# Optimization experiments

Hardware: AMD Instinct MI355X
Metric: run time of the kernel (lower is better)

Reference implementation:

```python
import jax, jax.numpy as jnp
import numpy as np

B, M, C, IMG, P, D, L, H, DFF, NC = 16, 4, 3, 224, 16, 768, 12, 12, 3072, 1000
G = IMG // P
S = G * G + 1
HD = D // H
EPS = 1e-6
SCALE = HD ** -0.5


def setup_inputs() -> dict:
    key = jax.random.key(0)
    ks = jax.random.split(key, 12)
    w = lambda k, shape: (jax.random.normal(k, shape) * 0.02).astype(jnp.float32)
    return {
        'x': jax.random.normal(ks[0], (B, C, IMG, IMG), jnp.float32),
        'x_tangent': jax.random.normal(ks[1], (B, M, C, IMG, IMG), jnp.float32),
        'patch_w': w(ks[2], (D, C * P * P)), 'patch_b': jnp.zeros((D,), jnp.float32),
        'cls_token': w(ks[3], (1, 1, D)), 'pos_embed': w(ks[4], (1, S, D)),
        'ln1_g': jnp.ones((L, D), jnp.float32), 'ln1_b': jnp.zeros((L, D), jnp.float32),
        'qkv_w': w(ks[5], (L, 3 * D, D)), 'qkv_b': jnp.zeros((L, 3 * D), jnp.float32),
        'proj_w': w(ks[6], (L, D, D)), 'proj_b': jnp.zeros((L, D), jnp.float32),
        'ln2_g': jnp.ones((L, D), jnp.float32), 'ln2_b': jnp.zeros((L, D), jnp.float32),
        'fc1_w': w(ks[7], (L, DFF, D)), 'fc1_b': jnp.zeros((L, DFF), jnp.float32),
        'fc2_w': w(ks[8], (L, D, DFF)), 'fc2_b': jnp.zeros((L, D), jnp.float32),
        'normf_g': jnp.ones((D,), jnp.float32), 'normf_b': jnp.zeros((D,), jnp.float32),
        'head_w': w(ks[9], (NC, D)), 'head_b': jnp.zeros((NC,), jnp.float32),
    }


def _patchify(img):
    # [b,C,IMG,IMG] -> [b, G*G, C*P*P], matching Conv2d(patch) weight layout (c, ph, pw)
    b = img.shape[0]
    p = img.reshape(b, C, G, P, G, P).transpose(0, 2, 4, 1, 3, 5)
    return p.reshape(b, G * G, C * P * P)


def _ln_jvp(x, t, g, b):
    # x: [B,S,D], t: [B,M,S,D]; params constant w.r.t. tangent directions
    mu = x.mean(-1, keepdims=True)
    xc = x - mu
    inv = jax.lax.rsqrt((xc * xc).mean(-1, keepdims=True) + EPS)
    xh = xc * inv
    y = xh * g + b
    xh_b, inv_b = xh[:, None], inv[:, None]
    ty = g * inv_b * (t - t.mean(-1, keepdims=True) - xh_b * (xh_b * t).mean(-1, keepdims=True))
    return y, ty


def _gelu_jvp(x, t):
    # exact (erf) GELU and its derivative; x: [B,S,F], t: [B,M,S,F]
    cdf = 0.5 * (1.0 + jax.lax.erf(x * 0.7071067811865476))
    pdf = jnp.exp(-0.5 * x * x) * 0.3989422804014327
    return x * cdf, t * (cdf + x * pdf)[:, None]


def _softmax_jvp(s, ts):
    # s: [B,H,S,S], ts: [B,M,H,S,S]
    a = jax.nn.softmax(s, axis=-1)
    a_b = a[:, None]
    ta = a_b * (ts - (a_b * ts).sum(-1, keepdims=True))
    return a, ta


def reference(x, x_tangent, patch_w, patch_b, cls_token, pos_embed,
              ln1_g, ln1_b, qkv_w, qkv_b, proj_w, proj_b, ln2_g, ln2_b,
              fc1_w, fc1_b, fc2_w, fc2_b, normf_g, normf_b, head_w, head_b):
    # patch embed (primal + tangent; bias/pos/cls are constants -> zero tangent)
    h = _patchify(x) @ patch_w.T + patch_b                                  # [B,N,D]
    th = (_patchify(x_tangent.reshape(B * M, C, IMG, IMG)) @ patch_w.T).reshape(B, M, G * G, D)
    cls = jnp.broadcast_to(cls_token, (B, 1, D))
    h = jnp.concatenate([cls, h], axis=1) + pos_embed                       # [B,S,D]
    th = jnp.concatenate([jnp.zeros((B, M, 1, D), th.dtype), th], axis=2)   # [B,M,S,D]

    for l in range(L):
        # --- attention (manual JVP, matching the torch einsum path) ---
        y, ty = _ln_jvp(h, th, ln1_g[l], ln1_b[l])
        qkv = y @ qkv_w[l].T + qkv_b[l]
        tqkv = ty @ qkv_w[l].T
        q, k, v = jnp.split(qkv, 3, axis=-1)
        tq, tk, tv = jnp.split(tqkv, 3, axis=-1)
        q = q.reshape(B, S, H, HD); k = k.reshape(B, S, H, HD); v = v.reshape(B, S, H, HD)
        tq = tq.reshape(B, M, S, H, HD); tk = tk.reshape(B, M, S, H, HD); tv = tv.reshape(B, M, S, H, HD)
        s = jnp.einsum('bqhd,bkhd->bhqk', q, k) * SCALE
        ts = (jnp.einsum('bmqhd,bkhd->bmhqk', tq, k)
              + jnp.einsum('bqhd,bmkhd->bmhqk', q, tk)) * SCALE
        a, ta = _softmax_jvp(s, ts)
        o = jnp.einsum('bhqk,bkhd->bqhd', a, v).reshape(B, S, D)
        to = (jnp.einsum('bmhqk,bkhd->bmqhd', ta, v)
              + jnp.einsum('bhqk,bmkhd->bmqhd', a, tv)).reshape(B, M, S, D)
        h = h + o @ proj_w[l].T + proj_b[l]
        th = th + to @ proj_w[l].T
        # --- mlp ---
        y, ty = _ln_jvp(h, th, ln2_g[l], ln2_b[l])
        y = y @ fc1_w[l].T + fc1_b[l]
        ty = ty @ fc1_w[l].T
        y, ty = _gelu_jvp(y, ty)
        h = h + y @ fc2_w[l].T + fc2_b[l]
        th = th + ty @ fc2_w[l].T

    y, ty = _ln_jvp(h, th, normf_g, normf_b)
    logits = y[:, 0] @ head_w.T + head_b            # token pooling
    tlogits = ty[:, :, 0] @ head_w.T                 # [B,M,NC]
    return logits, tlogits
```

## Files before the change

### kernel.cpp

```cpp
#include <hip/hip_runtime.h>
#include <hip/hip_bf16.h>

#define DEVI __device__ __forceinline__

typedef short  bf16x8 __attribute__((ext_vector_type(8)));
typedef float  f32x4  __attribute__((ext_vector_type(4)));

static constexpr int BB   = 16;
static constexpr int MM   = 4;
static constexpr int CC   = 3;
static constexpr int IMG  = 224;
static constexpr int PPP  = 16;
static constexpr int DD   = 768;
static constexpr int LL   = 12;
static constexpr int HH   = 12;
static constexpr int DFF  = 3072;
static constexpr int NCLS = 1000;
static constexpr int GG   = 14;
static constexpr int SS   = 197;
static constexpr int HD   = 64;
static constexpr int BT   = BB*SS;
static constexpr int BMT  = BB*MM*SS;
static constexpr int RT   = BT+BMT;
static constexpr int RP   = 15872;
static constexpr int SP   = 208;
static constexpr int QLD  = 3*DD;
static constexpr int PRP  = BB*GG*GG;
static constexpr int PRT  = (BB+BB*MM)*GG*GG;
static constexpr float EPSV  = 1e-6f;
static constexpr float SCALE = 0.125f;

static constexpr int NQW  = QLD*DD;
static constexpr int NPW  = DD*DD;
static constexpr int NF1W = DFF*DD;
static constexpr int NF2W = DD*DFF;
static constexpr int WTOT = NQW+NPW+NF1W+NF2W;

static constexpr int CH   = 4;
static constexpr int BMC  = (BB*MM)/CH;

DEVI unsigned short f2bf(float x){
  union { float f; unsigned u; } v; v.f = x;
  unsigned r = v.u + 0x7fffu + ((v.u>>16)&1u);
  return (unsigned short)(r>>16);
}
DEVI float bf2f(unsigned short x){
  union { unsigned u; float f; } v; v.u = ((unsigned)x)<<16;
  return v.f;
}
DEVI f32x4 mfma16(bf16x8 a, bf16x8 b, f32x4 c){
  return __builtin_amdgcn_mfma_f32_16x16x32_bf16(a,b,c,0,0,0);
}
typedef const void __attribute__((address_space(1)))* gas1;
typedef void __attribute__((address_space(3)))* las3;


__global__ __launch_bounds__(256) void f2bf_kernel(const float* __restrict__ in,
    unsigned short* __restrict__ out, size_t n){
  size_t i = (size_t)blockIdx.x*256 + threadIdx.x;
  size_t stride = (size_t)gridDim.x*256;
  for (; i<n; i+=stride) out[i] = f2bf(in[i]);
}

__global__ __launch_bounds__(256) void conv_layer(const float* __restrict__ qkvw,
    const float* __restrict__ projw, const float* __restrict__ f1w,
    const float* __restrict__ f2w, unsigned short* __restrict__ wl){
  int i = blockIdx.x*256 + threadIdx.x;
  float v;
  if (i < NQW)                v = qkvw[i];
  else if (i < NQW+NPW)       v = projw[i-NQW];
  else if (i < NQW+NPW+NF1W)  v = f1w[i-NQW-NPW];
  else                        v = f2w[i-NQW-NPW-NF1W];
  wl[i] = f2bf(v);
}

__global__ __launch_bounds__(256) void init_h(float* __restrict__ hh,
    const float* __restrict__ cls, const float* __restrict__ pos,
    const float* __restrict__ patch_b){
  size_t i = (size_t)blockIdx.x*256 + threadIdx.x;
  int r = (int)(i/DD), c = (int)(i%DD);
  float v = 0.f;
  if (r < BT){
    int s_ = r % SS;
    v = pos[(size_t)s_*DD + c] + (s_==0 ? cls[c] : patch_b[c]);
  }
  hh[i] = v;
}

__global__ __launch_bounds__(256) void patchify_k(const float* __restrict__ x,
    const float* __restrict__ xt, unsigned short* __restrict__ pat){
  size_t i = (size_t)blockIdx.x*256 + threadIdx.x;
  int r = (int)(i/DD), kk = (int)(i%DD);
  int c = kk>>8, rem = kk&255, py = rem>>4, px = rem&15;
  const float* src;
  if (r < PRP){
    int b_ = r/(GG*GG), p = r%(GG*GG);
    src = x + (((size_t)b_*CC + c)*IMG + (size_t)(p/GG)*PPP + py)*IMG + (p%GG)*PPP + px;
  } else {
    int rr = r-PRP; int bm = rr/(GG*GG), p = rr%(GG*GG);
    src = xt + (((size_t)bm*CC + c)*IMG + (size_t)(p/GG)*PPP + py)*IMG + (p%GG)*PPP + px;
  }
  pat[i] = f2bf(*src);
}


DEVI float blockSum256(float v, float* red){
  #pragma unroll
  for (int off=32; off; off>>=1) v += __shfl_xor(v, off, 64);
  int wave = threadIdx.x>>6;
  if ((threadIdx.x&63)==0) red[wave] = v;
  __syncthreads();
  float r = red[0]+red[1]+red[2]+red[3];
  __syncthreads();
  return r;
}

__global__ __launch_bounds__(256) void ln_primal(const float* __restrict__ hh,
    const float* __restrict__ g, const float* __restrict__ bb,
    unsigned short* __restrict__ ybf, float* __restrict__ stats){
  __shared__ float red[4];
  int r = blockIdx.x;
  const float* x = hh + (size_t)r*DD;
  int t = threadIdx.x;
  float x0=x[t], x1=x[t+256], x2=x[t+512];
  float mu = blockSum256(x0+x1+x2, red) * (1.f/DD);
  float d0=x0-mu, d1=x1-mu, d2=x2-mu;
  float var = blockSum256(d0*d0+d1*d1+d2*d2, red) * (1.f/DD);
  float inv = rsqrtf(var + EPSV);
  unsigned short* y = ybf + (size_t)r*DD;
  y[t]     = f2bf(d0*inv*g[t]     + bb[t]);
  y[t+256] = f2bf(d1*inv*g[t+256] + bb[t+256]);
  y[t+512] = f2bf(d2*inv*g[t+512] + bb[t+512]);
  if (t==0){ stats[2*r]=mu; stats[2*r+1]=inv; }
}

__global__ __launch_bounds__(256) void ln_tangent(const float* __restrict__ hh,
    const float* __restrict__ g, unsigned short* __restrict__ ybf,
    const float* __restrict__ stats){
  __shared__ float red[4];
  int r = blockIdx.x;
  int gr = BT + r;
  int s_ = r % SS;
  int b_ = (r / SS) / MM;
  int pr = b_*SS + s_;
  const float* tt = hh + (size_t)gr*DD;
  const float* xx = hh + (size_t)pr*DD;
  float mu = stats[2*pr], inv = stats[2*pr+1];
  int t = threadIdx.x;
  float t0=tt[t], t1=tt[t+256], t2=tt[t+512];
  float h0=(xx[t]-mu)*inv, h1=(xx[t+256]-mu)*inv, h2=(xx[t+512]-mu)*inv;
  float tmean = blockSum256(t0+t1+t2, red)*(1.f/DD);
  float dot   = blockSum256(h0*t0+h1*t1+h2*t2, red)*(1.f/DD);
  unsigned short* y = ybf + (size_t)gr*DD;
  y[t]     = f2bf(g[t]    *inv*(t0 - tmean - h0*dot));
  y[t+256] = f2bf(g[t+256]*inv*(t1 - tmean - h1*dot));
  y[t+512] = f2bf(g[t+512]*inv*(t2 - tmean - h2*dot));
}


template<int MODE>
__global__ __launch_bounds__(256,2) void gemm_bt(
    const unsigned short* __restrict__ A,
    const unsigned short* __restrict__ Aalt, int asplit, int lda,
    const unsigned short* __restrict__ W, int K, int N, int Mrows,
    float* __restrict__ outf, unsigned short* __restrict__ outb, int ldc,
    const float* __restrict__ bias, int bias_limit)
{
  __shared__ __attribute__((aligned(16))) unsigned short As[128*64];
  __shared__ __attribute__((aligned(16))) unsigned short Bs[128*64];
  const int tid = threadIdx.x;
  const int wave = tid>>6, lane = tid&63;
  const int tM = blockIdx.y, tN = blockIdx.x;
  f32x4 acc[4][4];
  f32x4 zf = {0.f,0.f,0.f,0.f};
  #pragma unroll
  for (int m=0;m<4;m++)
    #pragma unroll
    for (int n=0;n<4;n++) acc[m][n] = zf;
  const int wm = wave>>1, wn = wave&1;
  const int lrow = lane&15, lk8 = (lane>>4)<<3;
  const int srow = tid>>3;
  const int scol = (tid&7)<<3;
  const size_t arow0 = (size_t)tM*128;
  const size_t brow0 = (size_t)tN*128;

  for (int k0=0; k0<K; k0+=64){
    #pragma unroll
    for (int i=0;i<4;i++){
      int row = (int)arow0 + srow + i*32;
      const unsigned short* abase = (row < asplit) ? Aalt : A;
      const unsigned short* ga = abase + (size_t)row*lda + (k0+scol);
      __builtin_amdgcn_global_load_lds((gas1)ga, (las3)(As + i*2048 + wave*512), 16, 0, 0);
      const unsigned short* gb = W + (brow0+srow+i*32)*(size_t)K + (k0+scol);
      __builtin_amdgcn_global_load_lds((gas1)gb, (las3)(Bs + i*2048 + wave*512), 16, 0, 0);
    }
    __syncthreads();
    #pragma unroll
    for (int kk=0; kk<64; kk+=32){
      bf16x8 af[4], bw[4];
      #pragma unroll
      for (int m=0;m<4;m++) af[m] = *(const bf16x8*)(As + (wm*64+m*16+lrow)*64 + kk+lk8);
      #pragma unroll
      for (int n=0;n<4;n++) bw[n] = *(const bf16x8*)(Bs + (wn*64+n*16+lrow)*64 + kk+lk8);
      #pragma unroll
      for (int m=0;m<4;m++)
        #pragma unroll
        for (int n=0;n<4;n++)
          acc[m][n] = mfma16(af[m], bw[n], acc[m][n]);
    }
    __syncthreads();
  }

  const int colbase = tN*128 + wn*64 + lrow;
  const int rowbase = tM*128 + wm*64 + ((lane>>4)<<2);
  #pragma unroll
  for (int n=0;n<4;n++){
    int col = colbase + n*16;
    #pragma unroll
    for (int m=0;m<4;m++){
      #pragma unroll
      for (int i=0;i<4;i++){
        int r = rowbase + m*16 + i;
        float v = acc[m][n][i];
        if (MODE==0){
          if (r < bias_limit) v += bias[col];
          outb[(size_t)r*ldc + col] = f2bf(v);
        } else if (MODE==1){
          if (r < Mrows){
            if (r < bias_limit) v += bias[col];
            outf[(size_t)r*ldc + col] += v;
          }
        } else {
          if (r < PRT){
            int orow;
            if (r < PRP) orow = (r/196)*197 + 1 + r%196;
            else { int rr = r-PRP; orow = BT + (rr/196)*197 + 1 + rr%196; }
            outf[(size_t)orow*ldc + col] += v;
          }
        }
      }
    }
  }
}

__global__ __launch_bounds__(256) void transpose_v(const unsigned short* __restrict__ qkv,
    unsigned short* __restrict__ vT, unsigned short* __restrict__ tvT){
  __shared__ unsigned short tile[SP*65];
  int inst = blockIdx.x;
  size_t rowbase; unsigned short* dst; int h;
  if (inst < BB*HH){ int b_=inst/HH; h=inst%HH; rowbase=(size_t)b_*SS; dst = vT + (size_t)inst*HD*SP; }
  else { int i2=inst-BB*HH; int bm=i2/HH; h=i2%HH; rowbase=(size_t)BT+(size_t)bm*SS; dst = tvT + (size_t)i2*HD*SP; }
  int coff = 2*DD + h*HD;
  for (int i=threadIdx.x; i<SP*HD; i+=256){
    int k = i>>6, d = i&63;
    unsigned short v = (k<SS) ? qkv[(rowbase+k)*QLD + coff + d] : (unsigned short)0;
    tile[k*65+d] = v;
  }
  __syncthreads();
  for (int i=threadIdx.x; i<HD*SP; i+=256){
    int d = i/SP, k = i%SP;
    dst[(size_t)d*SP + k] = tile[k*65+d];
  }
}

__global__ __launch_bounds__(256) void attn_s1(const unsigned short* __restrict__ qkv,
                                               unsigned short* __restrict__ abf){
  int qt = blockIdx.x, inst = blockIdx.y;
  int wave = threadIdx.x>>6, lane = threadIdx.x&63;
  int lrow = lane&15, lk = (lane>>4)<<3;
  int q0 = qt*64 + wave*16;
  f32x4 acc[13];
  f32x4 zf = {0.f,0.f,0.f,0.f};
  #pragma unroll
  for (int n=0;n<13;n++) acc[n]=zf;
  int h = inst % HH, b_ = inst / HH;
  size_t prow = (size_t)b_*SS;
  const unsigned short* Ab = qkv + (prow + q0 + lrow)*QLD + h*HD + lk;
  const unsigned short* Bb = qkv + prow*QLD + DD + h*HD + lk;
  #pragma unroll
  for (int kk=0; kk<HD; kk+=32){
    bf16x8 av = *(const bf16x8*)(Ab + kk);
    #pragma unroll
    for (int n=0;n<13;n++){
      bf16x8 bv = *(const bf16x8*)(Bb + (size_t)(n*16+lrow)*QLD + kk);
      acc[n] = mfma16(av, bv, acc[n]);
    }
  }
  int grp = lane>>4;
  unsigned short* obase = abf + (size_t)inst*SP*SP;
  bool okc12 = (lrow < 5);
  #pragma unroll
  for (int i=0;i<4;i++){
    int qr = q0 + grp*4 + i;
    float val[13], e[13];
    float mv = -1e30f;
    #pragma unroll
    for (int n=0;n<13;n++){
      val[n] = acc[n][i]*SCALE;
      if (n<12 || okc12) mv = fmaxf(mv, val[n]);
    }
    #pragma unroll
    for (int off=8; off; off>>=1) mv = fmaxf(mv, __shfl_xor(mv, off, 64));
    float s = 0.f;
    #pragma unroll
    for (int n=0;n<13;n++){
      e[n] = (n<12 || okc12) ? __expf(val[n]-mv) : 0.f;
      s += e[n];
    }
    #pragma unroll
    for (int off=8; off; off>>=1) s += __shfl_xor(s, off, 64);
    float inv = 1.f/s;
    if (qr < SS){
      unsigned short* orow = obase + (size_t)qr*SP;
      #pragma unroll
      for (int n=0;n<13;n++) orow[n*16+lrow] = f2bf(e[n]*inv);
    }
  }
}

__global__ __launch_bounds__(256) void attn_s2(const unsigned short* __restrict__ qkv,
    const unsigned short* __restrict__ abf, unsigned short* __restrict__ tabf,
    int bmix0){
  int qt = blockIdx.x, il = blockIdx.y;
  int wave = threadIdx.x>>6, lane = threadIdx.x&63;
  int lrow = lane&15, lk = (lane>>4)<<3;
  int q0 = qt*64 + wave*16;
  f32x4 acc[13];
  f32x4 zf = {0.f,0.f,0.f,0.f};
  #pragma unroll
  for (int n=0;n<13;n++) acc[n]=zf;
  int h = il % HH;
  int bmix = bmix0 + il / HH;
  int b_ = bmix / MM;
  int bh = b_*HH + h;
  size_t prow = (size_t)b_*SS;
  size_t trow = (size_t)BT + (size_t)bmix*SS;
  #pragma unroll
  for (int p=0;p<2;p++){
    size_t ar = (p==0) ? trow : prow;
    size_t br = (p==1) ? trow : prow;
    const unsigned short* Ab = qkv + (ar + q0 + lrow)*QLD + h*HD + lk;
    const unsigned short* Bb = qkv + br*QLD + DD + h*HD + lk;
    #pragma unroll
    for (int kk=0; kk<HD; kk+=32){
      bf16x8 av = *(const bf16x8*)(Ab + kk);
      #pragma unroll
      for (int n=0;n<13;n++){
        bf16x8 bv = *(const bf16x8*)(Bb + (size_t)(n*16+lrow)*QLD + kk);
        acc[n] = mfma16(av, bv, acc[n]);
      }
    }
  }
  int grp = lane>>4;
  const unsigned short* abase = abf + (size_t)bh*SP*SP;
  unsigned short* tbase = tabf + (size_t)il*SP*SP;
  #pragma unroll
  for (int i=0;i<4;i++){
    int qr = q0 + grp*4 + i;
    int qc = (qr < SS) ? qr : (SS-1);
    const unsigned short* arow = abase + (size_t)qc*SP;
    float av[13], tv[13];
    float dot = 0.f;
    #pragma unroll
    for (int n=0;n<13;n++){
      tv[n] = acc[n][i]*SCALE;
      av[n] = bf2f(arow[n*16+lrow]);
      dot += av[n]*tv[n];
    }
    #pragma unroll
    for (int off=8; off; off>>=1) dot += __shfl_xor(dot, off, 64);
    if (qr < SS){
      unsigned short* trow_ = tbase + (size_t)qr*SP;
      #pragma unroll
      for (int n=0;n<13;n++) trow_[n*16+lrow] = f2bf(av[n]*(tv[n]-dot));
    }
  }
}

template<int NP>
__global__ __launch_bounds__(256) void attn_pv(
    const unsigned short* __restrict__ abf, const unsigned short* __restrict__ tabf,
    const unsigned short* __restrict__ vT,  const unsigned short* __restrict__ tvT,
    unsigned short* __restrict__ obf, int bmix0){
  int qt = blockIdx.x, il = blockIdx.y;
  int wave = threadIdx.x>>6, lane = threadIdx.x&63;
  int lrow = lane&15, lk = (lane>>4)<<3;
  int q0 = qt*64 + wave*16;
  int h = il % HH;
  int bmix = (NP==1) ? (il/HH) : (bmix0 + il/HH);
  int b_ = (NP==1) ? bmix : bmix/MM;
  int bh = b_*HH + h;
  f32x4 acc[4];
  f32x4 zf = {0.f,0.f,0.f,0.f};
  #pragma unroll
  for (int n=0;n<4;n++) acc[n]=zf;
  int arow = q0 + lrow; if (arow > SP-1) arow = SP-1;
  #pragma unroll
  for (int p=0;p<NP;p++){
    const unsigned short* Ab = (NP==2 && p==0) ? tabf + (size_t)il*SP*SP
                                               : abf + (size_t)bh*SP*SP;
    const unsigned short* Bb = (NP==2 && p==1) ? tvT + (size_t)(bmix*HH+h)*HD*SP
                                               : vT + (size_t)bh*HD*SP;
    #pragma unroll
    for (int ks=0; ks<6; ks++){
      int kb = ks*32 + lk;
      bf16x8 av = *(const bf16x8*)(Ab + (size_t)arow*SP + kb);
      #pragma unroll
      for (int n=0;n<4;n++){
        bf16x8 bv = *(const bf16x8*)(Bb + (size_t)(n*16+lrow)*SP + kb);
        acc[n] = mfma16(av, bv, acc[n]);
      }
    }
    {
      int kb = 192 + lk;
      const bf16x8 ZV = {0,0,0,0,0,0,0,0};
      bool ok = (lk < 16);
      bf16x8 av = ok ? *(const bf16x8*)(Ab + (size_t)arow*SP + kb) : ZV;
      #pragma unroll
      for (int n=0;n<4;n++){
        bf16x8 bv = ok ? *(const bf16x8*)(Bb + (size_t)(n*16+lrow)*SP + kb) : ZV;
        acc[n] = mfma16(av, bv, acc[n]);
      }
    }
  }
  size_t orow0 = (NP==1) ? (size_t)bmix*SS : (size_t)BT + (size_t)bmix*SS;
  int qr0 = q0 + ((lane>>4)<<2);
  #pragma unroll
  for (int n=0;n<4;n++){
    int cc = h*HD + n*16 + lrow;
    #pragma unroll
    for (int i=0;i<4;i++){
      int qr = qr0 + i;
      if (qr < SS) obf[(orow0+qr)*DD + cc] = f2bf(acc[n][i]);
    }
  }
}

__global__ __launch_bounds__(256) void gelu_k(unsigned short* __restrict__ fc1o,
                                              unsigned short* __restrict__ pgbf){
  int r = blockIdx.x;
  bool prim = r < BT;
  int pr = 0;
  if (!prim){ int idx = r-BT; int s_ = idx%SS; int b_ = (idx/SS)/MM; pr = b_*SS + s_; }
  size_t base  = (size_t)r*DFF;
  size_t pbase = (size_t)pr*DFF;
  for (int c=threadIdx.x; c<DFF; c+=256){
    if (prim){
      float x = bf2f(fc1o[base+c]);
      float cdf = 0.5f*(1.f + erff(x*0.70710678118654752f));
      pgbf[base+c] = f2bf(x*cdf);
    } else {
      float tv = bf2f(fc1o[base+c]);
      float x  = bf2f(fc1o[pbase+c]);
      float cdf = 0.5f*(1.f + erff(x*0.70710678118654752f));
      float pdf = __expf(-0.5f*x*x)*0.39894228040143267f;
      fc1o[base+c] = f2bf(tv*(cdf + x*pdf));
    }
  }
}

__global__ __launch_bounds__(256) void head_k(const unsigned short* __restrict__ ybf,
    const float* __restrict__ hw, const float* __restrict__ hb, float* __restrict__ out){
  __shared__ float ysh[DD];
  int ri = blockIdx.x;
  size_t yrow; float* o; bool wb;
  if (ri < BB){ yrow = (size_t)ri*SS; o = out + (size_t)ri*NCLS; wb = true; }
  else { int t2 = ri-BB; yrow = (size_t)BT + (size_t)t2*SS; o = out + (size_t)BB*NCLS + (size_t)t2*NCLS; wb = false; }
  for (int d=threadIdx.x; d<DD; d+=256) ysh[d] = bf2f(ybf[yrow*DD + d]);
  __syncthreads();
  for (int n=threadIdx.x; n<NCLS; n+=256){
    const float* wrow = hw + (size_t)n*DD;
    float acc = wb ? hb[n] : 0.f;
    for (int d=0; d<DD; d++) acc += ysh[d]*wrow[d];
    o[n] = acc;
  }
}

extern "C" void kernel_launch(void* const* d_in, const int* in_sizes, int n_in,
                              void* d_out, int out_size, void* d_ws, size_t ws_size,
                              hipStream_t stream)
{
  const float* x      = (const float*)d_in[0];
  const float* xt     = (const float*)d_in[1];
  const float* patch_w= (const float*)d_in[2];
  const float* patch_b= (const float*)d_in[3];
  const float* cls    = (const float*)d_in[4];
  const float* pos    = (const float*)d_in[5];
  const float* ln1_g  = (const float*)d_in[6];
  const float* ln1_b  = (const float*)d_in[7];
  const float* qkv_w  = (const float*)d_in[8];
  const float* qkv_b  = (const float*)d_in[9];
  const float* proj_w = (const float*)d_in[10];
  const float* proj_b = (const float*)d_in[11];
  const float* ln2_g  = (const float*)d_in[12];
  const float* ln2_b  = (const float*)d_in[13];
  const float* fc1_w  = (const float*)d_in[14];
  const float* fc1_b  = (const float*)d_in[15];
  const float* fc2_w  = (const float*)d_in[16];
  const float* fc2_b  = (const float*)d_in[17];
  const float* nf_g   = (const float*)d_in[18];
  const float* nf_b   = (const float*)d_in[19];
  const float* head_w = (const float*)d_in[20];
  const float* head_b = (const float*)d_in[21];
  float* out = (float*)d_out;

  char* ws = (char*)d_ws;
  size_t off = 0;
  auto alloc = [&](size_t bytes)->char*{
    char* p = ws + off;
    off = (off + bytes + 255) & ~(size_t)255;
    return p;
  };
  unsigned short* w_patch = (unsigned short*)alloc((size_t)DD*DD*2);
  unsigned short* wl      = (unsigned short*)alloc((size_t)WTOT*2);
  float* hh            = (float*)alloc((size_t)RP*DD*4);
  unsigned short* ybf  = (unsigned short*)alloc((size_t)RP*DD*2);
  float* stats         = (float*)alloc((size_t)BT*2*4);
  size_t slab0 = off;
  unsigned short* qkvbf= (unsigned short*)alloc((size_t)RP*QLD*2);
  unsigned short* vT   = (unsigned short*)alloc((size_t)BB*HH*HD*SP*2);
  unsigned short* tvT  = (unsigned short*)alloc((size_t)BB*MM*HH*HD*SP*2);
  unsigned short* abf  = (unsigned short*)alloc((size_t)BB*HH*SP*SP*2);
  unsigned short* tabf = (unsigned short*)alloc((size_t)BMC*HH*SP*SP*2);
  size_t endA = off;
  off = slab0;
  unsigned short* fc1o = (unsigned short*)alloc((size_t)RP*DFF*2);
  unsigned short* pgbf = (unsigned short*)alloc((size_t)BT*DFF*2);
  size_t endB = off;
  size_t need = (endA > endB) ? endA : endB;

  if (need > ws_size){
    hipMemsetAsync(d_out, 0x7f, (size_t)out_size*4, stream);
    return;
  }

  dim3 blk(256);
  f2bf_kernel<<<dim3(2304), blk, 0, stream>>>(patch_w, w_patch, (size_t)DD*DD);
  init_h<<<dim3((RP*DD)/256), blk, 0, stream>>>(hh, cls, pos, patch_b);
  patchify_k<<<dim3((PRT*DD)/256), blk, 0, stream>>>(x, xt, ybf);
  gemm_bt<2><<<dim3(DD/128, 123), blk, 0, stream>>>(ybf, nullptr, 0, DD, w_patch, DD, DD, PRT,
                                                    hh, nullptr, DD, nullptr, 0);

  unsigned short* w_qkv = wl;
  unsigned short* w_proj= wl + NQW;
  unsigned short* w_fc1 = wl + NQW + NPW;
  unsigned short* w_fc2 = wl + NQW + NPW + NF1W;

  for (int l=0; l<LL; l++){
    conv_layer<<<dim3(WTOT/256), blk, 0, stream>>>(qkv_w+(size_t)l*NQW, proj_w+(size_t)l*NPW,
                                                   fc1_w+(size_t)l*NF1W, fc2_w+(size_t)l*NF2W, wl);
    ln_primal <<<dim3(BT),  blk, 0, stream>>>(hh, ln1_g+(size_t)l*DD, ln1_b+(size_t)l*DD, ybf, stats);
    ln_tangent<<<dim3(BMT), blk, 0, stream>>>(hh, ln1_g+(size_t)l*DD, ybf, stats);
    gemm_bt<0><<<dim3(QLD/128, RP/128), blk, 0, stream>>>(ybf, nullptr, 0, DD, w_qkv,
        DD, QLD, RT, nullptr, qkvbf, QLD, qkv_b+(size_t)l*QLD, BT);
    transpose_v<<<dim3(BB*HH + BB*MM*HH), blk, 0, stream>>>(qkvbf, vT, tvT);
    attn_s1<<<dim3(4, BB*HH), blk, 0, stream>>>(qkvbf, abf);
    attn_pv<1><<<dim3(4, BB*HH), blk, 0, stream>>>(abf, nullptr, vT, nullptr, ybf, 0);
    for (int c=0; c<CH; c++){
      attn_s2<<<dim3(4, BMC*HH), blk, 0, stream>>>(qkvbf, abf, tabf, c*BMC);
      attn_pv<2><<<dim3(4, BMC*HH), blk, 0, stream>>>(abf, tabf, vT, tvT, ybf, c*BMC);
    }
    gemm_bt<1><<<dim3(DD/128, RP/128), blk, 0, stream>>>(ybf, nullptr, 0, DD, w_proj,
        DD, DD, RT, hh, nullptr, DD, proj_b+(size_t)l*DD, BT);
    ln_primal <<<dim3(BT),  blk, 0, stream>>>(hh, ln2_g+(size_t)l*DD, ln2_b+(size_t)l*DD, ybf, stats);
    ln_tangent<<<dim3(BMT), blk, 0, stream>>>(hh, ln2_g+(size_t)l*DD, ybf, stats);
    gemm_bt<0><<<dim3(DFF/128, RP/128), blk, 0, stream>>>(ybf, nullptr, 0, DD, w_fc1,
        DD, DFF, RT, nullptr, fc1o, DFF, fc1_b+(size_t)l*DFF, BT);
    gelu_k<<<dim3(RT), blk, 0, stream>>>(fc1o, pgbf);
    gemm_bt<1><<<dim3(DD/128, RP/128), blk, 0, stream>>>(fc1o, pgbf, BT, DFF, w_fc2,
        DFF, DD, RT, hh, nullptr, DD, fc2_b+(size_t)l*DD, BT);
  }

  ln_primal <<<dim3(BT),  blk, 0, stream>>>(hh, nf_g, nf_b, ybf, stats);
  ln_tangent<<<dim3(BMT), blk, 0, stream>>>(hh, nf_g, ybf, stats);
  head_k<<<dim3(BB + BB*MM), blk, 0, stream>>>(ybf, head_w, head_b, out);
}
```

Measured before the change: 8.521 ms.

## Fuse layernorm kernels, convert all weights upfront, remap GEMM tiles per XCD, vectorize GELU

Primal and tangent layernorm are merged into one launch that recomputes the primal statistics per row with a single four-way block reduction, so the stats buffer and the second launch go away. All layers' weights are converted to bf16 in one kernel when the workspace is large enough, so the per-layer conversion launch is skipped. GEMM workgroup IDs are remapped so that consecutive tiles land on the same XCD, which is meant to improve L2 reuse. GELU is vectorized to 8-wide bf16 accesses, and the final layernorm only processes the rows the head reads. The one-pass variance (E[x^2] - mu^2) is less numerically robust, and converting every layer's weights up front takes more workspace memory.

```diff
diff --git a/kernel.cpp b/kernel.cpp
--- a/kernel.cpp
+++ b/kernel.cpp
@@ -74,6 +74,19 @@
   wl[i] = f2bf(v);
 }
 
+__global__ __launch_bounds__(256) void conv_all(const float* __restrict__ qkvw,
+    const float* __restrict__ projw, const float* __restrict__ f1w,
+    const float* __restrict__ f2w, unsigned short* __restrict__ wl){
+  int l = blockIdx.y;
+  int i = blockIdx.x*256 + threadIdx.x;
+  float v;
+  if (i < NQW)                v = qkvw[(size_t)l*NQW + i];
+  else if (i < NQW+NPW)       v = projw[(size_t)l*NPW + (i-NQW)];
+  else if (i < NQW+NPW+NF1W)  v = f1w[(size_t)l*NF1W + (i-NQW-NPW)];
+  else                        v = f2w[(size_t)l*NF2W + (i-NQW-NPW-NF1W)];
+  wl[(size_t)l*WTOT + i] = f2bf(v);
+}
+
 __global__ __launch_bounds__(256) void init_h(float* __restrict__ hh,
     const float* __restrict__ cls, const float* __restrict__ pos,
     const float* __restrict__ patch_b){
@@ -104,57 +117,99 @@
 }
 
 
-DEVI float blockSum256(float v, float* red){
-  #pragma unroll
-  for (int off=32; off; off>>=1) v += __shfl_xor(v, off, 64);
-  int wave = threadIdx.x>>6;
-  if ((threadIdx.x&63)==0) red[wave] = v;
+DEVI void blockSum4(float&a,float&b,float&c,float&d,float* red){
+  #pragma unroll
+  for (int off=32; off; off>>=1){
+    a += __shfl_xor(a,off,64); b += __shfl_xor(b,off,64);
+    c += __shfl_xor(c,off,64); d += __shfl_xor(d,off,64);
+  }
+  int w = threadIdx.x>>6;
+  if ((threadIdx.x&63)==0){ red[w]=a; red[4+w]=b; red[8+w]=c; red[12+w]=d; }
   __syncthreads();
-  float r = red[0]+red[1]+red[2]+red[3];
+  a = red[0]+red[1]+red[2]+red[3];
+  b = red[4]+red[5]+red[6]+red[7];
+  c = red[8]+red[9]+red[10]+red[11];
+  d = red[12]+red[13]+red[14]+red[15];
   __syncthreads();
-  return r;
-}
-
-__global__ __launch_bounds__(256) void ln_primal(const float* __restrict__ hh,
+}
+
+__global__ __launch_bounds__(256) void ln_fused(const float* __restrict__ hh,
     const float* __restrict__ g, const float* __restrict__ bb,
-    unsigned short* __restrict__ ybf, float* __restrict__ stats){
-  __shared__ float red[4];
+    unsigned short* __restrict__ ybf){
+  __shared__ float red[16];
   int r = blockIdx.x;
-  const float* x = hh + (size_t)r*DD;
   int t = threadIdx.x;
-  float x0=x[t], x1=x[t+256], x2=x[t+512];
-  float mu = blockSum256(x0+x1+x2, red) * (1.f/DD);
-  float d0=x0-mu, d1=x1-mu, d2=x2-mu;
-  float var = blockSum256(d0*d0+d1*d1+d2*d2, red) * (1.f/DD);
-  float inv = rsqrtf(var + EPSV);
   unsigned short* y = ybf + (size_t)r*DD;
-  y[t]     = f2bf(d0*inv*g[t]     + bb[t]);
-  y[t+256] = f2bf(d1*inv*g[t+256] + bb[t+256]);
-  y[t+512] = f2bf(d2*inv*g[t+512] + bb[t+512]);
-  if (t==0){ stats[2*r]=mu; stats[2*r+1]=inv; }
-}
-
-__global__ __launch_bounds__(256) void ln_tangent(const float* __restrict__ hh,
-    const float* __restrict__ g, unsigned short* __restrict__ ybf,
-    const float* __restrict__ stats){
-  __shared__ float red[4];
-  int r = blockIdx.x;
-  int gr = BT + r;
-  int s_ = r % SS;
-  int b_ = (r / SS) / MM;
-  int pr = b_*SS + s_;
-  const float* tt = hh + (size_t)gr*DD;
-  const float* xx = hh + (size_t)pr*DD;
-  float mu = stats[2*pr], inv = stats[2*pr+1];
+  if (r < BT){
+    const float* x = hh + (size_t)r*DD;
+    float x0=x[t], x1=x[t+256], x2=x[t+512];
+    float s1=x0+x1+x2, s2=x0*x0+x1*x1+x2*x2, s3=0.f, s4=0.f;
+    blockSum4(s1,s2,s3,s4,red);
+    float mu  = s1*(1.f/DD);
+    float inv = rsqrtf(s2*(1.f/DD) - mu*mu + EPSV);
+    y[t]     = f2bf((x0-mu)*inv*g[t]     + bb[t]);
+    y[t+256] = f2bf((x1-mu)*inv*g[t+256] + bb[t+256]);
+    y[t+512] = f2bf((x2-mu)*inv*g[t+512] + bb[t+512]);
+  } else {
+    int idx = r-BT;
+    int s_ = idx % SS;
+    int b_ = (idx / SS) / MM;
+    int pr = b_*SS + s_;
+    const float* tt = hh + (size_t)r*DD;
+    const float* xx = hh + (size_t)pr*DD;
+    float t0=tt[t], t1=tt[t+256], t2=tt[t+512];
+    float x0=xx[t], x1=xx[t+256], x2=xx[t+512];
+    float s1=x0+x1+x2, s2=x0*x0+x1*x1+x2*x2;
+    float s3=t0+t1+t2, s4=x0*t0+x1*t1+x2*t2;
+    blockSum4(s1,s2,s3,s4,red);
+    float mu  = s1*(1.f/DD);
+    float inv = rsqrtf(s2*(1.f/DD) - mu*mu + EPSV);
+    float tmean = s3*(1.f/DD);
+    float dot   = inv*(s4*(1.f/DD) - mu*tmean);
+    y[t]     = f2bf(g[t]    *inv*(t0 - tmean - (x0-mu)*inv*dot));
+    y[t+256] = f2bf(g[t+256]*inv*(t1 - tmean - (x1-mu)*inv*dot));
+    y[t+512] = f2bf(g[t+512]*inv*(t2 - tmean - (x2-mu)*inv*dot));
+  }
+}
+
+__global__ __launch_bounds__(256) void ln_head(const float* __restrict__ hh,
+    const float* __restrict__ g, const float* __restrict__ bb,
+    unsigned short* __restrict__ ybf){
+  __shared__ float red[16];
+  int ri = blockIdx.x;
   int t = threadIdx.x;
-  float t0=tt[t], t1=tt[t+256], t2=tt[t+512];
-  float h0=(xx[t]-mu)*inv, h1=(xx[t+256]-mu)*inv, h2=(xx[t+512]-mu)*inv;
-  float tmean = blockSum256(t0+t1+t2, red)*(1.f/DD);
-  float dot   = blockSum256(h0*t0+h1*t1+h2*t2, red)*(1.f/DD);
-  unsigned short* y = ybf + (size_t)gr*DD;
-  y[t]     = f2bf(g[t]    *inv*(t0 - tmean - h0*dot));
-  y[t+256] = f2bf(g[t+256]*inv*(t1 - tmean - h1*dot));
-  y[t+512] = f2bf(g[t+512]*inv*(t2 - tmean - h2*dot));
+  if (ri < BB){
+    size_t row = (size_t)ri*SS;
+    const float* x = hh + row*DD;
+    float x0=x[t], x1=x[t+256], x2=x[t+512];
+    float s1=x0+x1+x2, s2=x0*x0+x1*x1+x2*x2, s3=0.f, s4=0.f;
+    blockSum4(s1,s2,s3,s4,red);
+    float mu  = s1*(1.f/DD);
+    float inv = rsqrtf(s2*(1.f/DD) - mu*mu + EPSV);
+    unsigned short* y = ybf + row*DD;
+    y[t]     = f2bf((x0-mu)*inv*g[t]     + bb[t]);
+    y[t+256] = f2bf((x1-mu)*inv*g[t+256] + bb[t+256]);
+    y[t+512] = f2bf((x2-mu)*inv*g[t+512] + bb[t+512]);
+  } else {
+    int t2 = ri - BB;
+    size_t row = (size_t)BT + (size_t)t2*SS;
+    size_t prow = (size_t)(t2/MM)*SS;
+    const float* tt = hh + row*DD;
+    const float* xx = hh + prow*DD;
+    float t0=tt[t], t1=tt[t+256], t2v=tt[t+512];
+    float x0=xx[t], x1=xx[t+256], x2=xx[t+512];
+    float s1=x0+x1+x2, s2=x0*x0+x1*x1+x2*x2;
+    float s3=t0+t1+t2v, s4=x0*t0+x1*t1+x2*t2v;
+    blockSum4(s1,s2,s3,s4,red);
+    float mu  = s1*(1.f/DD);
+    float inv = rsqrtf(s2*(1.f/DD) - mu*mu + EPSV);
+    float tmean = s3*(1.f/DD);
+    float dot   = inv*(s4*(1.f/DD) - mu*tmean);
+    unsigned short* y = ybf + row*DD;
+    y[t]     = f2bf(g[t]    *inv*(t0  - tmean - (x0-mu)*inv*dot));
+    y[t+256] = f2bf(g[t+256]*inv*(t1  - tmean - (x1-mu)*inv*dot));
+    y[t+512] = f2bf(g[t+512]*inv*(t2v - tmean - (x2-mu)*inv*dot));
+  }
 }
 
 
@@ -170,7 +225,12 @@
   __shared__ __attribute__((aligned(16))) unsigned short Bs[128*64];
   const int tid = threadIdx.x;
   const int wave = tid>>6, lane = tid&63;
-  const int tM = blockIdx.y, tN = blockIdx.x;
+  const int nwg  = gridDim.x*gridDim.y;
+  const int orig = blockIdx.y*gridDim.x + blockIdx.x;
+  const int xcd = orig & 7, i8 = orig >> 3;
+  const int qq = nwg >> 3, rr_ = nwg & 7;
+  const int wg = (xcd < rr_ ? xcd*(qq+1) : rr_*(qq+1) + (xcd-rr_)*qq) + i8;
+  const int tN = wg % gridDim.x, tM = wg / gridDim.x;
   f32x4 acc[4][4];
   f32x4 zf = {0.f,0.f,0.f,0.f};
   #pragma unroll
@@ -442,19 +502,33 @@
   bool prim = r < BT;
   int pr = 0;
   if (!prim){ int idx = r-BT; int s_ = idx%SS; int b_ = (idx/SS)/MM; pr = b_*SS + s_; }
-  size_t base  = (size_t)r*DFF;
-  size_t pbase = (size_t)pr*DFF;
-  for (int c=threadIdx.x; c<DFF; c+=256){
+  bf16x8* base = (bf16x8*)(fc1o + (size_t)r*DFF);
+  const bf16x8* pb = (const bf16x8*)(fc1o + (size_t)pr*DFF);
+  bf16x8* pg = (bf16x8*)(pgbf + (size_t)r*DFF);
+  for (int c = threadIdx.x; c < DFF/8; c += 256){
     if (prim){
-      float x = bf2f(fc1o[base+c]);
-      float cdf = 0.5f*(1.f + erff(x*0.70710678118654752f));
-      pgbf[base+c] = f2bf(x*cdf);
+      bf16x8 xv = base[c];
+      bf16x8 o;
+      #pragma unroll
+      for (int j=0;j<8;j++){
+        float x = bf2f((unsigned short)xv[j]);
+        float cdf = 0.5f*(1.f + erff(x*0.70710678118654752f));
+        o[j] = (short)f2bf(x*cdf);
+      }
+      pg[c] = o;
     } else {
-      float tv = bf2f(fc1o[base+c]);
-      float x  = bf2f(fc1o[pbase+c]);
-      float cdf = 0.5f*(1.f + erff(x*0.70710678118654752f));
-      float pdf = __expf(-0.5f*x*x)*0.39894228040143267f;
-      fc1o[base+c] = f2bf(tv*(cdf + x*pdf));
+      bf16x8 tv8 = base[c];
+      bf16x8 xv  = pb[c];
+      bf16x8 o;
+      #pragma unroll
+      for (int j=0;j<8;j++){
+        float x  = bf2f((unsigned short)xv[j]);
+        float tv = bf2f((unsigned short)tv8[j]);
+        float cdf = 0.5f*(1.f + erff(x*0.70710678118654752f));
+        float pdf = __expf(-0.5f*x*x)*0.39894228040143267f;
+        o[j] = (short)f2bf(tv*(cdf + x*pdf));
+      }
+      base[c] = o;
     }
   }
 }
@@ -511,23 +585,31 @@
     off = (off + bytes + 255) & ~(size_t)255;
     return p;
   };
-  unsigned short* w_patch = (unsigned short*)alloc((size_t)DD*DD*2);
-  unsigned short* wl      = (unsigned short*)alloc((size_t)WTOT*2);
-  float* hh            = (float*)alloc((size_t)RP*DD*4);
-  unsigned short* ybf  = (unsigned short*)alloc((size_t)RP*DD*2);
-  float* stats         = (float*)alloc((size_t)BT*2*4);
-  size_t slab0 = off;
-  unsigned short* qkvbf= (unsigned short*)alloc((size_t)RP*QLD*2);
-  unsigned short* vT   = (unsigned short*)alloc((size_t)BB*HH*HD*SP*2);
-  unsigned short* tvT  = (unsigned short*)alloc((size_t)BB*MM*HH*HD*SP*2);
-  unsigned short* abf  = (unsigned short*)alloc((size_t)BB*HH*SP*SP*2);
-  unsigned short* tabf = (unsigned short*)alloc((size_t)BMC*HH*SP*SP*2);
-  size_t endA = off;
-  off = slab0;
-  unsigned short* fc1o = (unsigned short*)alloc((size_t)RP*DFF*2);
-  unsigned short* pgbf = (unsigned short*)alloc((size_t)BT*DFF*2);
-  size_t endB = off;
-  size_t need = (endA > endB) ? endA : endB;
+
+  unsigned short *w_patch, *wl, *ybf, *qkvbf, *vT, *tvT, *abf, *tabf, *fc1o, *pgbf;
+  float *hh;
+  auto layout = [&](bool allw)->size_t{
+    off = 0;
+    w_patch = (unsigned short*)alloc((size_t)DD*DD*2);
+    wl      = (unsigned short*)alloc((size_t)WTOT*2*(allw?LL:1));
+    hh      = (float*)alloc((size_t)RP*DD*4);
+    ybf     = (unsigned short*)alloc((size_t)RP*DD*2);
+    size_t slab0 = off;
+    qkvbf = (unsigned short*)alloc((size_t)RP*QLD*2);
+    vT    = (unsigned short*)alloc((size_t)BB*HH*HD*SP*2);
+    tvT   = (unsigned short*)alloc((size_t)BB*MM*HH*HD*SP*2);
+    abf   = (unsigned short*)alloc((size_t)BB*HH*SP*SP*2);
+    tabf  = (unsigned short*)alloc((size_t)BMC*HH*SP*SP*2);
+    size_t endA = off;
+    off = slab0;
+    fc1o = (unsigned short*)alloc((size_t)RP*DFF*2);
+    pgbf = (unsigned short*)alloc((size_t)BT*DFF*2);
+    size_t endB = off;
+    return (endA > endB) ? endA : endB;
+  };
+  size_t needAll = layout(true);
+  bool allw = (needAll <= ws_size);
+  size_t need = allw ? needAll : layout(false);
 
   if (need > ws_size){
     hipMemsetAsync(d_out, 0x7f, (size_t)out_size*4, stream);
@@ -536,21 +618,23 @@
 
   dim3 blk(256);
   f2bf_kernel<<<dim3(2304), blk, 0, stream>>>(patch_w, w_patch, (size_t)DD*DD);
+  if (allw)
+    conv_all<<<dim3(WTOT/256, LL), blk, 0, stream>>>(qkv_w, proj_w, fc1_w, fc2_w, wl);
   init_h<<<dim3((RP*DD)/256), blk, 0, stream>>>(hh, cls, pos, patch_b);
   patchify_k<<<dim3((PRT*DD)/256), blk, 0, stream>>>(x, xt, ybf);
   gemm_bt<2><<<dim3(DD/128, 123), blk, 0, stream>>>(ybf, nullptr, 0, DD, w_patch, DD, DD, PRT,
                                                     hh, nullptr, DD, nullptr, 0);
 
-  unsigned short* w_qkv = wl;
-  unsigned short* w_proj= wl + NQW;
-  unsigned short* w_fc1 = wl + NQW + NPW;
-  unsigned short* w_fc2 = wl + NQW + NPW + NF1W;
-
   for (int l=0; l<LL; l++){
-    conv_layer<<<dim3(WTOT/256), blk, 0, stream>>>(qkv_w+(size_t)l*NQW, proj_w+(size_t)l*NPW,
-                                                   fc1_w+(size_t)l*NF1W, fc2_w+(size_t)l*NF2W, wl);
-    ln_primal <<<dim3(BT),  blk, 0, stream>>>(hh, ln1_g+(size_t)l*DD, ln1_b+(size_t)l*DD, ybf, stats);
-    ln_tangent<<<dim3(BMT), blk, 0, stream>>>(hh, ln1_g+(size_t)l*DD, ybf, stats);
+    if (!allw)
+      conv_layer<<<dim3(WTOT/256), blk, 0, stream>>>(qkv_w+(size_t)l*NQW, proj_w+(size_t)l*NPW,
+                                                     fc1_w+(size_t)l*NF1W, fc2_w+(size_t)l*NF2W, wl);
+    const unsigned short* w_qkv = wl + (allw ? (size_t)l*WTOT : 0);
+    const unsigned short* w_proj= w_qkv + NQW;
+    const unsigned short* w_fc1 = w_qkv + NQW + NPW;
+    const unsigned short* w_fc2 = w_qkv + NQW + NPW + NF1W;
+
+    ln_fused<<<dim3(RT), blk, 0, stream>>>(hh, ln1_g+(size_t)l*DD, ln1_b+(size_t)l*DD, ybf);
     gemm_bt<0><<<dim3(QLD/128, RP/128), blk, 0, stream>>>(ybf, nullptr, 0, DD, w_qkv,
         DD, QLD, RT, nullptr, qkvbf, QLD, qkv_b+(size_t)l*QLD, BT);
     transpose_v<<<dim3(BB*HH + BB*MM*HH), blk, 0, stream>>>(qkvbf, vT, tvT);
@@ -562,8 +646,7 @@
     }
     gemm_bt<1><<<dim3(DD/128, RP/128), blk, 0, stream>>>(ybf, nullptr, 0, DD, w_proj,
         DD, DD, RT, hh, nullptr, DD, proj_b+(size_t)l*DD, BT);
-    ln_primal <<<dim3(BT),  blk, 0, stream>>>(hh, ln2_g+(size_t)l*DD, ln2_b+(size_t)l*DD, ybf, stats);
-    ln_tangent<<<dim3(BMT), blk, 0, stream>>>(hh, ln2_g+(size_t)l*DD, ybf, stats);
+    ln_fused<<<dim3(RT), blk, 0, stream>>>(hh, ln2_g+(size_t)l*DD, ln2_b+(size_t)l*DD, ybf);
     gemm_bt<0><<<dim3(DFF/128, RP/128), blk, 0, stream>>>(ybf, nullptr, 0, DD, w_fc1,
         DD, DFF, RT, nullptr, fc1o, DFF, fc1_b+(size_t)l*DFF, BT);
     gelu_k<<<dim3(RT), blk, 0, stream>>>(fc1o, pgbf);
@@ -571,7 +654,6 @@
         DFF, DD, RT, hh, nullptr, DD, fc2_b+(size_t)l*DD, BT);
   }
 
-  ln_primal <<<dim3(BT),  blk, 0, stream>>>(hh, nf_g, nf_b, ybf, stats);
-  ln_tangent<<<dim3(BMT), blk, 0, stream>>>(hh, nf_g, ybf, stats);
+  ln_head<<<dim3(BB + BB*MM), blk, 0, stream>>>(hh, nf_g, nf_b, ybf);
   head_k<<<dim3(BB + BB*MM), blk, 0, stream>>>(ybf, head_w, head_b, out);
 }
```

New measurement: 8.995 ms. 1.06x slower.
